# Performance work log

Hardware: AMD Instinct MI355X
Metric: run time of the kernel (lower is better)

Reference implementation:

```python
import jax, jax.numpy as jnp
import numpy as np


def setup_inputs() -> dict:
    key = jax.random.key(0)
    k1, k2 = jax.random.split(key)
    T, J, d = 16384, 64, 1024
    h = jax.random.normal(k1, (1, T, d), dtype=jnp.float32)
    s = jax.random.normal(k2, (T, J), dtype=jnp.float32)
    return {"h": h, "s": s}


def reference(h, s):
    # z1 = max over query axis, b = softmax over context positions  [T]
    b = jax.nn.softmax(jnp.max(s, axis=-1))
    # weighted sum of context vectors: sum_t b[t] * h[0, t, :]  -> [d]
    ctx = jnp.einsum('t,td->d', b, h[0])
    # tile the attended vector across all T positions -> [d, T]
    T = s.shape[0]
    q2c = jnp.broadcast_to(ctx[:, None], (ctx.shape[0], T))
    return q2c
```

## Files before the change

### kernel.cpp

```cpp
#include <hip/hip_runtime.h>
#include <math.h>

#define T_DIM 16384
#define J_DIM 64
#define D_DIM 1024

#define E_OFF    0
#define BMAX_OFF 16384
#define BSUM_OFF 16448
#define INVZ_OFF 16512
#define CTX_OFF  16640
#define PART_OFF 17664

#define CTX_BLOCKS   512
#define ROWS_PER_BLK 32

__global__ __launch_bounds__(256) void k1_rowmax(const float* __restrict__ s,
                                                 float* __restrict__ ws) {
    __shared__ float red[256];
    const int tid = threadIdx.x;
    const int t = blockIdx.x * 256 + tid;
    const float4* s4 = (const float4*)s + (size_t)t * (J_DIM / 4);
    float m = -INFINITY;
#pragma unroll
    for (int j = 0; j < J_DIM / 4; ++j) {
        float4 v = s4[j];
        m = fmaxf(m, fmaxf(fmaxf(v.x, v.y), fmaxf(v.z, v.w)));
    }
    ws[E_OFF + t] = m;
    red[tid] = m;
    __syncthreads();
    for (int off = 128; off > 0; off >>= 1) {
        if (tid < off) red[tid] = fmaxf(red[tid], red[tid + off]);
        __syncthreads();
    }
    if (tid == 0) ws[BMAX_OFF + blockIdx.x] = red[0];
    if (blockIdx.x < D_DIM / 256) ws[CTX_OFF + blockIdx.x * 256 + tid] = 0.0f;
}

__global__ __launch_bounds__(256) void k2_exp(float* __restrict__ ws) {
    __shared__ float red[256];
    const int tid = threadIdx.x;
    red[tid] = (tid < 64) ? ws[BMAX_OFF + tid] : -INFINITY;
    __syncthreads();
    for (int off = 128; off > 0; off >>= 1) {
        if (tid < off) red[tid] = fmaxf(red[tid], red[tid + off]);
        __syncthreads();
    }
    const float M = red[0];
    __syncthreads();
    const int t = blockIdx.x * 256 + tid;
    const float e = expf(ws[E_OFF + t] - M);
    ws[E_OFF + t] = e;
    red[tid] = e;
    __syncthreads();
    for (int off = 128; off > 0; off >>= 1) {
        if (tid < off) red[tid] += red[tid + off];
        __syncthreads();
    }
    if (tid == 0) ws[BSUM_OFF + blockIdx.x] = red[0];
}

__global__ __launch_bounds__(256) void k3_partial(const float* __restrict__ h,
                                                  float* __restrict__ ws) {
    __shared__ float w[ROWS_PER_BLK];
    const int tid = threadIdx.x;
    const int b = blockIdx.x;
    if (tid < ROWS_PER_BLK) w[tid] = ws[E_OFF + b * ROWS_PER_BLK + tid];
    __syncthreads();
    const float4* h4 = (const float4*)h;
    float4 acc = make_float4(0.f, 0.f, 0.f, 0.f);
    const size_t base = (size_t)b * ROWS_PER_BLK * (D_DIM / 4) + tid;
#pragma unroll 8
    for (int r = 0; r < ROWS_PER_BLK; ++r) {
        const float4 v = h4[base + (size_t)r * (D_DIM / 4)];
        const float wt = w[r];
        acc.x = fmaf(wt, v.x, acc.x);
        acc.y = fmaf(wt, v.y, acc.y);
        acc.z = fmaf(wt, v.z, acc.z);
        acc.w = fmaf(wt, v.w, acc.w);
    }
    ((float4*)(ws + PART_OFF))[(size_t)b * (D_DIM / 4) + tid] = acc;
}

__global__ __launch_bounds__(256) void k4_reduce(float* __restrict__ ws) {
    __shared__ float red[64];
    const int tid = threadIdx.x;
    if (blockIdx.x == 0) {
        if (tid < 64) red[tid] = ws[BSUM_OFF + tid];
        __syncthreads();
        for (int off = 32; off > 0; off >>= 1) {
            if (tid < off) red[tid] += red[tid + off];
            __syncthreads();
        }
        if (tid == 0) ws[INVZ_OFF] = 1.0f / red[0];
    }
    const int pc = blockIdx.x >> 2;
    const int dd = (blockIdx.x & 3) * 256 + tid;
    const float* part = ws + PART_OFF;
    float sum = 0.f;
#pragma unroll 8
    for (int p = pc * 32; p < pc * 32 + 32; ++p) sum += part[(size_t)p * D_DIM + dd];
    atomicAdd(&ws[CTX_OFF + dd], sum);
}

__global__ __launch_bounds__(256) void k5_broadcast(const float* __restrict__ ws,
                                                    float4* __restrict__ out4) {
    const int dd = blockIdx.x >> 4;
    const float v = ws[CTX_OFF + dd] * ws[INVZ_OFF];
    const size_t idx = (size_t)blockIdx.x * 256 + threadIdx.x;
    out4[idx] = make_float4(v, v, v, v);
}

extern "C" void kernel_launch(void* const* d_in, const int* in_sizes, int n_in,
                              void* d_out, int out_size, void* d_ws, size_t ws_size,
                              hipStream_t stream) {
    const float* h = (const float*)d_in[0];
    const float* s = (const float*)d_in[1];
    float* ws = (float*)d_ws;
    float4* out = (float4*)d_out;

    k1_rowmax<<<T_DIM / 256, 256, 0, stream>>>(s, ws);
    k2_exp<<<T_DIM / 256, 256, 0, stream>>>(ws);
    k3_partial<<<CTX_BLOCKS, 256, 0, stream>>>(h, ws);
    k4_reduce<<<64, 256, 0, stream>>>(ws);
    k5_broadcast<<<((size_t)D_DIM * T_DIM / 4) / 256, 256, 0, stream>>>(ws, out);
}
```

Before: 125.5 us.

## Fuse softmax into partial sums using per-block online max rescaling

Replaces the five-kernel pipeline with two kernels. The first computes row maxima, a block-local max and a block-local exp sum, then accumulates the weighted partial context for its 32 rows, all in one pass. The second rescales the block partials by exp(blockmax - globalmax), reduces them across blocks, and writes the broadcast output row for its dimension. This removes three launches, the atomics and the intermediate exp buffer, at the cost of redundant global-max and Z reductions in every one of the 1024 output blocks and strided partial reads.

```diff
diff --git a/kernel.cpp b/kernel.cpp
--- a/kernel.cpp
+++ b/kernel.cpp
@@ -5,111 +5,114 @@
 #define J_DIM 64
 #define D_DIM 1024
 
-#define E_OFF    0
-#define BMAX_OFF 16384
-#define BSUM_OFF 16448
-#define INVZ_OFF 16512
-#define CTX_OFF  16640
-#define PART_OFF 17664
+#define NB   512
+#define RPB  32
 
-#define CTX_BLOCKS   512
-#define ROWS_PER_BLK 32
+#define MB_OFF   0
+#define ZB_OFF   512
+#define PART_OFF 1024
 
-__global__ __launch_bounds__(256) void k1_rowmax(const float* __restrict__ s,
-                                                 float* __restrict__ ws) {
-    __shared__ float red[256];
-    const int tid = threadIdx.x;
-    const int t = blockIdx.x * 256 + tid;
-    const float4* s4 = (const float4*)s + (size_t)t * (J_DIM / 4);
-    float m = -INFINITY;
-#pragma unroll
-    for (int j = 0; j < J_DIM / 4; ++j) {
-        float4 v = s4[j];
-        m = fmaxf(m, fmaxf(fmaxf(v.x, v.y), fmaxf(v.z, v.w)));
-    }
-    ws[E_OFF + t] = m;
-    red[tid] = m;
-    __syncthreads();
-    for (int off = 128; off > 0; off >>= 1) {
-        if (tid < off) red[tid] = fmaxf(red[tid], red[tid + off]);
-        __syncthreads();
-    }
-    if (tid == 0) ws[BMAX_OFF + blockIdx.x] = red[0];
-    if (blockIdx.x < D_DIM / 256) ws[CTX_OFF + blockIdx.x * 256 + tid] = 0.0f;
-}
-
-__global__ __launch_bounds__(256) void k2_exp(float* __restrict__ ws) {
-    __shared__ float red[256];
-    const int tid = threadIdx.x;
-    red[tid] = (tid < 64) ? ws[BMAX_OFF + tid] : -INFINITY;
-    __syncthreads();
-    for (int off = 128; off > 0; off >>= 1) {
-        if (tid < off) red[tid] = fmaxf(red[tid], red[tid + off]);
-        __syncthreads();
-    }
-    const float M = red[0];
-    __syncthreads();
-    const int t = blockIdx.x * 256 + tid;
-    const float e = expf(ws[E_OFF + t] - M);
-    ws[E_OFF + t] = e;
-    red[tid] = e;
-    __syncthreads();
-    for (int off = 128; off > 0; off >>= 1) {
-        if (tid < off) red[tid] += red[tid + off];
-        __syncthreads();
-    }
-    if (tid == 0) ws[BSUM_OFF + blockIdx.x] = red[0];
-}
-
-__global__ __launch_bounds__(256) void k3_partial(const float* __restrict__ h,
-                                                  float* __restrict__ ws) {
-    __shared__ float w[ROWS_PER_BLK];
+__global__ __launch_bounds__(256) void kb_heavy(const float* __restrict__ h,
+                                                const float* __restrict__ s,
+                                                float* __restrict__ ws) {
+    __shared__ float rowmax[RPB];
+    __shared__ float wts[RPB];
     const int tid = threadIdx.x;
     const int b = blockIdx.x;
-    if (tid < ROWS_PER_BLK) w[tid] = ws[E_OFF + b * ROWS_PER_BLK + tid];
+
+    const float4* s4 = (const float4*)s + (size_t)b * (RPB * J_DIM / 4);
+    float4 v0 = s4[tid];
+    float4 v1 = s4[tid + 256];
+    float m0 = fmaxf(fmaxf(v0.x, v0.y), fmaxf(v0.z, v0.w));
+    float m1 = fmaxf(fmaxf(v1.x, v1.y), fmaxf(v1.z, v1.w));
+#pragma unroll
+    for (int off = 1; off < 16; off <<= 1) {
+        m0 = fmaxf(m0, __shfl_xor(m0, off));
+        m1 = fmaxf(m1, __shfl_xor(m1, off));
+    }
+    if ((tid & 15) == 0) {
+        rowmax[tid >> 4] = m0;
+        rowmax[16 + (tid >> 4)] = m1;
+    }
     __syncthreads();
+
+    if (tid == 0) {
+        float Mb = rowmax[0];
+#pragma unroll
+        for (int r = 1; r < RPB; ++r) Mb = fmaxf(Mb, rowmax[r]);
+        float Zb = 0.f;
+#pragma unroll
+        for (int r = 0; r < RPB; ++r) {
+            const float w = expf(rowmax[r] - Mb);
+            wts[r] = w;
+            Zb += w;
+        }
+        ws[MB_OFF + b] = Mb;
+        ws[ZB_OFF + b] = Zb;
+    }
+    __syncthreads();
+
     const float4* h4 = (const float4*)h;
     float4 acc = make_float4(0.f, 0.f, 0.f, 0.f);
-    const size_t base = (size_t)b * ROWS_PER_BLK * (D_DIM / 4) + tid;
+    const size_t base = (size_t)b * (RPB * D_DIM / 4) + tid;
 #pragma unroll 8
-    for (int r = 0; r < ROWS_PER_BLK; ++r) {
+    for (int r = 0; r < RPB; ++r) {
         const float4 v = h4[base + (size_t)r * (D_DIM / 4)];
-        const float wt = w[r];
+        const float wt = wts[r];
         acc.x = fmaf(wt, v.x, acc.x);
         acc.y = fmaf(wt, v.y, acc.y);
         acc.z = fmaf(wt, v.z, acc.z);
         acc.w = fmaf(wt, v.w, acc.w);
     }
+
     ((float4*)(ws + PART_OFF))[(size_t)b * (D_DIM / 4) + tid] = acc;
 }
 
-__global__ __launch_bounds__(256) void k4_reduce(float* __restrict__ ws) {
-    __shared__ float red[64];
+__global__ __launch_bounds__(256) void kcd_reduce_bcast(const float* __restrict__ ws,
+                                                        float4* __restrict__ out4) {
+    __shared__ float redm[256];
+    __shared__ float redz[256];
+    __shared__ float redc[256];
     const int tid = threadIdx.x;
-    if (blockIdx.x == 0) {
-        if (tid < 64) red[tid] = ws[BSUM_OFF + tid];
+    const int dd = blockIdx.x;
+
+    const float m0 = ws[MB_OFF + tid];
+    const float m1 = ws[MB_OFF + tid + 256];
+    const float* prow = ws + PART_OFF + (size_t)tid * D_DIM + dd;
+    const float p0 = prow[0];
+    const float p1 = prow[(size_t)256 * D_DIM];
+    const float z0 = ws[ZB_OFF + tid];
+    const float z1 = ws[ZB_OFF + tid + 256];
+
+    redm[tid] = fmaxf(m0, m1);
+    __syncthreads();
+#pragma unroll
+    for (int off = 128; off > 0; off >>= 1) {
+        if (tid < off) redm[tid] = fmaxf(redm[tid], redm[tid + off]);
         __syncthreads();
-        for (int off = 32; off > 0; off >>= 1) {
-            if (tid < off) red[tid] += red[tid + off];
-            __syncthreads();
+    }
+    const float M = redm[0];
+
+    const float s0 = expf(m0 - M);
+    const float s1 = expf(m1 - M);
+    redz[tid] = s0 * z0 + s1 * z1;
+    redc[tid] = s0 * p0 + s1 * p1;
+    __syncthreads();
+#pragma unroll
+    for (int off = 128; off > 0; off >>= 1) {
+        if (tid < off) {
+            redz[tid] += redz[tid + off];
+            redc[tid] += redc[tid + off];
         }
-        if (tid == 0) ws[INVZ_OFF] = 1.0f / red[0];
+        __syncthreads();
     }
-    const int pc = blockIdx.x >> 2;
-    const int dd = (blockIdx.x & 3) * 256 + tid;
-    const float* part = ws + PART_OFF;
-    float sum = 0.f;
-#pragma unroll 8
-    for (int p = pc * 32; p < pc * 32 + 32; ++p) sum += part[(size_t)p * D_DIM + dd];
-    atomicAdd(&ws[CTX_OFF + dd], sum);
-}
+    const float val = redc[0] / redz[0];
 
-__global__ __launch_bounds__(256) void k5_broadcast(const float* __restrict__ ws,
-                                                    float4* __restrict__ out4) {
-    const int dd = blockIdx.x >> 4;
-    const float v = ws[CTX_OFF + dd] * ws[INVZ_OFF];
-    const size_t idx = (size_t)blockIdx.x * 256 + threadIdx.x;
-    out4[idx] = make_float4(v, v, v, v);
+    const float4 v4 = make_float4(val, val, val, val);
+    float4* o = out4 + (size_t)dd * (T_DIM / 4);
+#pragma unroll
+    for (int i = 0; i < T_DIM / 4 / 256; ++i)
+        o[(size_t)i * 256 + tid] = v4;
 }
 
 extern "C" void kernel_launch(void* const* d_in, const int* in_sizes, int n_in,
@@ -120,9 +123,6 @@
     float* ws = (float*)d_ws;
     float4* out = (float4*)d_out;
 
-    k1_rowmax<<<T_DIM / 256, 256, 0, stream>>>(s, ws);
-    k2_exp<<<T_DIM / 256, 256, 0, stream>>>(ws);
-    k3_partial<<<CTX_BLOCKS, 256, 0, stream>>>(h, ws);
-    k4_reduce<<<64, 256, 0, stream>>>(ws);
-    k5_broadcast<<<((size_t)D_DIM * T_DIM / 4) / 256, 256, 0, stream>>>(ws, out);
+    kb_heavy<<<NB, 256, 0, stream>>>(h, s, ws);
+    kcd_reduce_bcast<<<D_DIM, 256, 0, stream>>>(ws, out);
 }
```

After: 117.9 us. 6.0% less time.
